# Kernel tuning notes

Hardware: AMD Instinct MI355X
Metric: run time of the kernel (lower is better)

## Reference

```python
import jax, jax.numpy as jnp
import numpy as np
from jax import lax

B, G, D, S = 1, 2048, 64, 2
H_FULL = 200
H0 = H_FULL // 2 ** (S - 1)
PC_RANGE = (-50.0, -50.0, -4.0, 50.0, 50.0, 4.0)
THRESH = 0.05
CHUNK = 128


def conv3x3(x, w):
    # x: [b,c,h,w], w: [o,i,3,3]
    return lax.conv_general_dilated(x, w, (1, 1), 'SAME',
                                    dimension_numbers=('NCHW', 'OIHW', 'NCHW'))


def instance_norm(x, eps=1e-5):
    mu = x.mean(axis=(2, 3), keepdims=True)
    var = x.var(axis=(2, 3), keepdims=True)
    return (x - mu) / jnp.sqrt(var + eps)


def basic_block(x, w1, w2):
    # conv-(BN@init=identity)-relu-conv-(BN)-add-relu
    h = jax.nn.relu(conv3x3(x, w1))
    h = conv3x3(h, w2)
    return jax.nn.relu(x + h)


def upsampling_add(x, skip, w):
    b, c, h, wd = x.shape
    xu = jax.image.resize(x, (b, c, 2 * h, 2 * wd), method='bilinear')
    xu = instance_norm(conv3x3(xu, w))
    return xu + skip


def render_stage(means, cov6, feats, opac, mask, H, W):
    # Orthographic BEV splatting (3DGS-style EWA + front-to-back compositing).
    g, d = feats.shape
    sh = H / 100.0
    sw = W / 100.0
    # full_proj_transform: px = -sh*y + H/2 ; py = -sw*x + W/2
    u = -sh * means[:, 1] + 0.5 * H
    v = -sw * means[:, 0] + 0.5 * W
    # cov2d = J Sigma J^T + 0.3*I, J = [[0,-sh,0],[-sw,0,0]]
    a = sh * sh * cov6[:, 3] + 0.3
    c = sw * sw * cov6[:, 0] + 0.3
    bb = sh * sw * cov6[:, 1]
    det = jnp.maximum(a * c - bb * bb, 1e-8)
    A = c / det
    Bc = -bb / det
    C = a / det
    xs = jnp.arange(W, dtype=jnp.float32)
    ys = jnp.arange(H, dtype=jnp.float32)
    nc = g // CHUNK

    def step(carry, inp):
        T, out = carry
        u_, v_, A_, B_, C_, op_, mk_, ft_ = inp
        dx = u_[:, None, None] - xs[None, None, :]
        dy = v_[:, None, None] - ys[None, :, None]
        power = (-0.5 * (A_[:, None, None] * dx * dx + C_[:, None, None] * dy * dy)
                 - B_[:, None, None] * dx * dy)
        alpha = jnp.minimum(op_[:, None, None] * jnp.exp(power), 0.99)
        alpha = jnp.where((alpha >= 1.0 / 255.0) & mk_[:, None, None] & (power <= 0.0),
                          alpha, 0.0)
        cp = jnp.cumprod(1.0 - alpha, axis=0)
        t_exc = jnp.concatenate([jnp.ones_like(cp[:1]), cp[:-1]], 0) * T
        out = out + jnp.einsum('ghw,gd->dhw', alpha * t_exc, ft_)
        return (T * cp[-1], out), None

    ch = lambda arr: arr.reshape(nc, CHUNK, *arr.shape[1:])
    init = (jnp.ones((H, W), jnp.float32), jnp.zeros((d, H, W), jnp.float32))
    (_, out), _ = lax.scan(step, init,
                           (ch(u), ch(v), ch(A), ch(Bc), ch(C), ch(opac), ch(mask), ch(feats)))
    return out  # bg color = 0


def setup_inputs() -> dict:
    key = jax.random.key(0)
    ks = jax.random.split(key, 10)
    features = jax.random.normal(ks[0], (B, G, D), jnp.float32)
    xy = jax.random.uniform(ks[1], (B, G, 2), jnp.float32, -55.0, 55.0)
    z = jax.random.uniform(ks[2], (B, G, 1), jnp.float32, -5.0, 5.0)
    means3D = jnp.concatenate([xy, z], -1)
    L = jax.random.normal(ks[3], (B, G, 3, 3), jnp.float32) * 0.5
    Sig = jnp.einsum('bgij,bgkj->bgik', L, L) + 0.1 * jnp.eye(3, dtype=jnp.float32)
    cov3D = jnp.stack([Sig[..., 0, 0], Sig[..., 0, 1], Sig[..., 0, 2],
                       Sig[..., 1, 1], Sig[..., 1, 2], Sig[..., 2, 2]], -1)
    opacities = jax.random.uniform(ks[4], (B, G, S), jnp.float32)
    w_scale = 1.0 / np.sqrt(D * 9)
    bev_emb = jax.random.normal(ks[5], (H0 * H0, D), jnp.float32) * 0.02
    conv1_w = jax.random.normal(ks[6], (S, D, D, 3, 3), jnp.float32) * w_scale
    blk_w = jax.random.normal(ks[7], (S, 2, 2, D, D, 3, 3), jnp.float32) * w_scale
    up_w = jax.random.normal(ks[8], (S - 1, D, D, 3, 3), jnp.float32) * w_scale
    return {'features': features, 'means3D': means3D, 'cov3D': cov3D,
            'opacities': opacities, 'bev_emb': bev_emb, 'conv1_w': conv1_w,
            'blk_w': blk_w, 'up_w': up_w}


def reference(features, means3D, cov3D, opacities, bev_emb, conv1_w, blk_w, up_w):
    b = features.shape[0]
    d = features.shape[-1]
    m = means3D
    mask_pos = ((m[..., 0] >= PC_RANGE[0]) & (m[..., 0] <= PC_RANGE[3]) &
                (m[..., 1] >= PC_RANGE[1]) & (m[..., 1] <= PC_RANGE[4]) &
                (m[..., 2] >= PC_RANGE[2]) & (m[..., 2] <= PC_RANGE[5]))
    num_g = jnp.float32(0.0)
    bevs = []
    for s in range(S):
        H = H0 * 2 ** s
        mask = (opacities[..., s] > THRESH) & mask_pos
        rend = jax.vmap(lambda mn, cv, ft, op, mk: render_stage(mn, cv, ft, op, mk, H, H))
        bevs.append(rend(means3D, cov3D, features, opacities[..., s], mask))
        num_g = num_g + jnp.mean(jnp.sum(mask.astype(jnp.float32), 1))
    x = jnp.broadcast_to(jnp.transpose(bev_emb.reshape(H0, H0, d), (2, 0, 1))[None],
                         (b, d, H0, H0))
    for s in range(S):
        bev = conv3x3(bevs[s], conv1_w[s])
        if s == 0:
            x = x + bev
        else:
            x = upsampling_add(x, bev, up_w[s - 1])
        for blk in range(2):
            x = basic_block(x, blk_w[s, blk, 0], blk_w[s, blk, 1])
    return x, num_g
```

## Files before the change

### kernel.cpp

```cpp
#include <hip/hip_runtime.h>
#include <math.h>

#define G_N 2048
#define CCH 256
#define PSTR 12
#define NBLK 1024
#define WC (64 * 64 * 9)

typedef short bhalf8 __attribute__((ext_vector_type(8)));
typedef float f32x4 __attribute__((ext_vector_type(4)));
typedef unsigned short u16;

__device__ __forceinline__ u16 f2bf(float f) {
    unsigned u = __float_as_uint(f);
    unsigned r = (u + 0x7fffu + ((u >> 16) & 1u)) >> 16;
    return (u16)r;
}
__device__ __forceinline__ float b2f(u16 h) {
    return __uint_as_float((unsigned)h << 16);
}

__device__ __forceinline__ ushort4 chload4(const u16* p) {
    unsigned long long u = __hip_atomic_load((const unsigned long long*)p,
        __ATOMIC_RELAXED, __HIP_MEMORY_SCOPE_AGENT);
    union { unsigned long long u; ushort4 s; } x; x.u = u;
    return x.s;
}
__device__ __forceinline__ void chstore4(u16* p, ushort4 v) {
    union { unsigned long long u; ushort4 s; } x; x.s = v;
    __hip_atomic_store((unsigned long long*)p, x.u,
                       __ATOMIC_RELAXED, __HIP_MEMORY_SCOPE_AGENT);
}
__device__ __forceinline__ void cstore8(float* p, float a, float b) {
    union { unsigned long long u; float f[2]; } x;
    x.f[0] = a; x.f[1] = b;
    __hip_atomic_store((unsigned long long*)p, x.u,
                       __ATOMIC_RELAXED, __HIP_MEMORY_SCOPE_AGENT);
}
__device__ __forceinline__ float cload(const float* p) {
    return __hip_atomic_load(p, __ATOMIC_RELAXED, __HIP_MEMORY_SCOPE_AGENT);
}

__device__ __forceinline__ void gbar(int* leaf, int* root, int* flag, int phase) {
    asm volatile("s_waitcnt vmcnt(0) lgkmcnt(0)" ::: "memory");
    __syncthreads();
    if (threadIdx.x == 0) {
        int g = blockIdx.x >> 5;
        int old = atomicAdd(&leaf[g * 16], 1);
        if ((old & 31) == 31) {
            int o2 = atomicAdd(root, 1);
            if ((o2 & 31) == 31)
                __hip_atomic_store(flag, phase, __ATOMIC_RELAXED,
                                   __HIP_MEMORY_SCOPE_AGENT);
        }
        while (__hip_atomic_load(flag, __ATOMIC_RELAXED,
                                 __HIP_MEMORY_SCOPE_AGENT) < phase)
            __builtin_amdgcn_s_sleep(16);
    }
    __syncthreads();
    asm volatile("" ::: "memory");
}

__device__ __forceinline__ void render_tile(
    int unit, const float* __restrict__ params, const int* __restrict__ counts,
    const float* __restrict__ feats, u16* __restrict__ out0,
    u16* __restrict__ out1, char* smem)
{
    int s = (unit < 169) ? 0 : 1;
    int t = (s == 0) ? unit : unit - 169;
    int tw = (s == 0) ? 13 : 25;
    int bxx = t % tw, byy = t / tw;
    int H = 100 << s;
    const float* P = params + s * G_N * PSTR;
    u16* out = s ? out1 : out0;
    int cnt = counts[s];

    float* raw = (float*)smem;
    float* cmp = raw + CCH * PSTR;
    int* s_wsum = (int*)(smem + 24576);

    int tid = threadIdx.x;
    int w = tid >> 6, lane = tid & 63;
    int pxl = lane & 7, pyl = lane >> 3;
    int x0 = bxx * 8, y0 = byy * 8;
    int px = x0 + pxl, py = y0 + pyl;
    bool active = (px < H) && (py < H);
    float fx = (float)px, fy = (float)py;
    float tx0 = (float)x0, tx1 = (float)min(H - 1, x0 + 7);
    float ty0 = (float)y0, ty1 = (float)min(H - 1, y0 + 7);

    f32x4 acc[4];
#pragma unroll
    for (int k = 0; k < 4; ++k) acc[k] = (f32x4){0.f, 0.f, 0.f, 0.f};
    float T = 1.f;

    for (int base = 0; base < cnt; base += CCH) {
        int anyalive = __syncthreads_or((int)(active && T > 1e-6f));
        if (!anyalive) break;
        int n = min(CCH, cnt - base);
        for (int i = tid; i < n * 3; i += 256)
            ((float4*)raw)[i] = ((const float4*)(P + base * PSTR))[i];
        __syncthreads();
        bool pass = false;
        if (tid < n) {
            float u = raw[tid * PSTR + 0], v = raw[tid * PSTR + 1];
            float rx = raw[tid * PSTR + 8], ry = raw[tid * PSTR + 9];
            pass = (u + rx >= tx0) && (u - rx <= tx1) &&
                   (v + ry >= ty0) && (v - ry <= ty1);
        }
        unsigned long long bal = __ballot(pass);
        int prefix = __popcll(bal & ((1ull << lane) - 1ull));
        if (lane == 0) s_wsum[w] = __popcll(bal);
        __syncthreads();
        int woff = 0;
        for (int k = 0; k < 4; ++k) if (k < w) woff += s_wsum[k];
        if (pass) {
            float4* dst = (float4*)(cmp + (woff + prefix) * PSTR);
            const float4* src = (const float4*)(raw + tid * PSTR);
            dst[0] = src[0]; dst[1] = src[1]; dst[2] = src[2];
        }
        __syncthreads();
        int nc = s_wsum[0] + s_wsum[1] + s_wsum[2] + s_wsum[3];
        if (active && T > 1e-6f) {
            for (int j = 0; j < nc; ++j) {
                float4 q0 = *(const float4*)(cmp + j * PSTR);
                float4 q1 = *(const float4*)(cmp + j * PSTR + 4);
                float dx = q0.x - fx, dy = q0.y - fy;
                float power = -0.5f * (q0.z * dx * dx + q1.x * dy * dy) - q0.w * dx * dy;
                if (power <= 0.f && power >= q1.z) {
                    float alpha = fminf(q1.y * __expf(power), 0.99f);
                    float wgt = alpha * T;
                    const f32x4* f4 = (const f32x4*)(feats + __float_as_int(q1.w) * 64) + w * 4;
#pragma unroll
                    for (int k = 0; k < 4; ++k) {
                        f32x4 fv = f4[k];
                        acc[k][0] = fmaf(wgt, fv[0], acc[k][0]);
                        acc[k][1] = fmaf(wgt, fv[1], acc[k][1]);
                        acc[k][2] = fmaf(wgt, fv[2], acc[k][2]);
                        acc[k][3] = fmaf(wgt, fv[3], acc[k][3]);
                    }
                    T *= (1.f - alpha);
                }
            }
        }
    }

    __syncthreads();
    float* shf = (float*)smem;
#pragma unroll
    for (int k = 0; k < 4; ++k)
        *(float4*)&shf[lane * 68 + w * 16 + k * 4] =
            (float4){acc[k][0], acc[k][1], acc[k][2], acc[k][3]};
    __syncthreads();
    for (int j = tid; j < 1024; j += 256) {
        int lp = j >> 4, c4 = (j & 15) * 4;
        int gy = y0 + (lp >> 3), gx = x0 + (lp & 7);
        if (gy < H && gx < H) {
            float4 v = *(float4*)&shf[lp * 68 + c4];
            ushort4 o = { f2bf(v.x), f2bf(v.y), f2bf(v.z), f2bf(v.w) };
            chstore4(&out[((gy * H + gx) << 6) + c4], o);
        }
    }
}

__device__ __forceinline__ void conv_tile(
    int bx, int H, const u16* __restrict__ in, const u16* __restrict__ wp,
    const float* __restrict__ bev, u16* __restrict__ outb,
    int ups, int dostats, float* __restrict__ sacc, char* smem)
{
    u16* xlds = (u16*)smem;
    u16* fin  = (u16*)(smem + 14400);
    float* red = (float*)(smem + 16384 + 8704);

    int tid = threadIdx.x;
    int gw = (H + 7) >> 3;
    int by = bx / gw, bxx = bx - by * gw;
    int y0 = by * 8, x0 = bxx * 8;
    int w = tid >> 6, lane = tid & 63;
    int n = lane & 15, q = lane >> 4;
    int Hh = H >> 1;
    int oy = (y0 >> 1) - 2, ox = (x0 >> 1) - 2;

    if (ups) {
        for (int i = tid; i < 1024; i += 256) {
            int px = i >> 4, c4 = (i & 15) * 4;
            int iy = px >> 3, ix = px & 7;
            int gyi = oy + iy, gxi = ox + ix;
            ushort4 v = {0, 0, 0, 0};
            if (gyi >= 0 && gyi < Hh && gxi >= 0 && gxi < Hh)
                v = chload4(&in[((gyi * Hh + gxi) << 6) + c4]);
            *(ushort4*)&fin[px * 68 + c4] = v;
        }
        __syncthreads();
    }

    for (int i = tid; i < 1600; i += 256) {
        int px = i >> 4, c4 = (i & 15) * 4;
        int yy = px / 10, xx = px - yy * 10;
        int gy = y0 - 1 + yy, gx = x0 - 1 + xx;
        ushort4 v = {0, 0, 0, 0};
        if (gy >= 0 && gy < H && gx >= 0 && gx < H) {
            if (ups) {
                int yi = gy >> 1, xi = gx >> 1;
                int yb = (gy & 1) ? min(yi + 1, Hh - 1) : max(yi - 1, 0);
                int xb = (gx & 1) ? min(xi + 1, Hh - 1) : max(xi - 1, 0);
                int t0 = yi - oy, t1 = xi - ox, t2 = yb - oy, t3 = xb - ox;
                ushort4 f00 = *(const ushort4*)&fin[(t0 * 8 + t1) * 68 + c4];
                ushort4 f01 = *(const ushort4*)&fin[(t0 * 8 + t3) * 68 + c4];
                ushort4 f10 = *(const ushort4*)&fin[(t2 * 8 + t1) * 68 + c4];
                ushort4 f11 = *(const ushort4*)&fin[(t2 * 8 + t3) * 68 + c4];
                v.x = f2bf(0.5625f * b2f(f00.x) + 0.1875f * (b2f(f01.x) + b2f(f10.x)) + 0.0625f * b2f(f11.x));
                v.y = f2bf(0.5625f * b2f(f00.y) + 0.1875f * (b2f(f01.y) + b2f(f10.y)) + 0.0625f * b2f(f11.y));
                v.z = f2bf(0.5625f * b2f(f00.z) + 0.1875f * (b2f(f01.z) + b2f(f10.z)) + 0.0625f * b2f(f11.z));
                v.w = f2bf(0.5625f * b2f(f00.w) + 0.1875f * (b2f(f01.w) + b2f(f10.w)) + 0.0625f * b2f(f11.w));
            } else {
                v = chload4(&in[((gy * H + gx) << 6) + c4]);
            }
        }
        *(ushort4*)&xlds[px * 72 + c4] = v;
    }
    __syncthreads();

    f32x4 acc[4];
#pragma unroll
    for (int m = 0; m < 4; ++m) acc[m] = (f32x4){0.f, 0.f, 0.f, 0.f};
    const bhalf8* wp8 = (const bhalf8*)wp;
    int sy = 2 * w + (n >> 3), sx = n & 7;

    bhalf8 a0 = wp8[0 * 64 + lane];
    bhalf8 a1 = wp8[1 * 64 + lane];
    bhalf8 a2 = wp8[2 * 64 + lane];
    bhalf8 a3 = wp8[3 * 64 + lane];
    bhalf8 bb = *(const bhalf8*)&xlds[(sy * 10 + sx) * 72 + q * 8];

#pragma unroll 1
    for (int p = 0; p < 18; ++p) {
        bhalf8 na0, na1, na2, na3, nbb;
        if (p < 17) {
            int pn = p + 1;
            na0 = wp8[(pn * 4 + 0) * 64 + lane];
            na1 = wp8[(pn * 4 + 1) * 64 + lane];
            na2 = wp8[(pn * 4 + 2) * 64 + lane];
            na3 = wp8[(pn * 4 + 3) * 64 + lane];
            int tap = pn >> 1, ch = pn & 1;
            int dy = tap / 3, dx = tap - dy * 3;
            nbb = *(const bhalf8*)&xlds[((sy + dy) * 10 + sx + dx) * 72 + ch * 32 + q * 8];
        }
        acc[0] = __builtin_amdgcn_mfma_f32_16x16x32_bf16(a0, bb, acc[0], 0, 0, 0);
        acc[1] = __builtin_amdgcn_mfma_f32_16x16x32_bf16(a1, bb, acc[1], 0, 0, 0);
        acc[2] = __builtin_amdgcn_mfma_f32_16x16x32_bf16(a2, bb, acc[2], 0, 0, 0);
        acc[3] = __builtin_amdgcn_mfma_f32_16x16x32_bf16(a3, bb, acc[3], 0, 0, 0);
        a0 = na0; a1 = na1; a2 = na2; a3 = na3; bb = nbb;
    }

    int gy = y0 + sy, gx = x0 + sx;
    if (gy < H && gx < H) {
        int base = (gy * H + gx) << 6;
#pragma unroll
        for (int m = 0; m < 4; ++m) {
            int oc0 = m * 16 + q * 4;
            float v0 = acc[m][0], v1 = acc[m][1], v2 = acc[m][2], v3 = acc[m][3];
            if (bev) {
                float4 av = *(const float4*)&bev[base + oc0];
                v0 += av.x; v1 += av.y; v2 += av.z; v3 += av.w;
            }
            ushort4 o = { f2bf(v0), f2bf(v1), f2bf(v2), f2bf(v3) };
            chstore4(&outb[base + oc0], o);
        }
    }

    if (dostats) {
#pragma unroll
        for (int m = 0; m < 4; ++m)
#pragma unroll
            for (int r = 0; r < 4; ++r) {
                float v = acc[m][r];
                float s = v, s2 = v * v;
#pragma unroll
                for (int d = 1; d < 16; d <<= 1) {
                    s += __shfl_xor(s, d, 64);
                    s2 += __shfl_xor(s2, d, 64);
                }
                if (n == 0) {
                    int oc = m * 16 + q * 4 + r;
                    red[w * 128 + oc] = s;
                    red[w * 128 + 64 + oc] = s2;
                }
            }
        __syncthreads();
        if (tid < 128) {
            float t = red[tid] + red[128 + tid] + red[256 + tid] + red[384 + tid];
            atomicAdd(&sacc[tid], t);
        }
    }
}

__device__ __forceinline__ void bb_tile(
    int bx, int H, const u16* __restrict__ in,
    const u16* __restrict__ wp1, const u16* __restrict__ wp2,
    u16* __restrict__ outb, float* __restrict__ outf, int final_,
    int nrm, const u16* __restrict__ nskip, const float* __restrict__ sraw,
    char* smem)
{
    u16* xin  = (u16*)smem;
    u16* ilds = (u16*)(smem + 20736);
    float* nm = (float*)(smem + 35136);
    float* nr = nm + 64;

    int tid = threadIdx.x;
    int gw = (H + 7) >> 3;
    int by = bx / gw, bxx = bx - by * gw;
    int y0 = by * 8, x0 = bxx * 8;
    int w = tid >> 6, lane = tid & 63;
    int n = lane & 15, q = lane >> 4;

    if (nrm) {
        if (tid < 64) {
            float s = cload(&sraw[tid]), s2 = cload(&sraw[64 + tid]);
            float mean = s * (1.f / 40000.f);
            float var = s2 * (1.f / 40000.f) - mean * mean;
            nm[tid] = mean;
            nr[tid] = rsqrtf(var + 1e-5f);
        }
        __syncthreads();
    }

    for (int i = tid; i < 2304; i += 256) {
        int px = i >> 4, c4 = (i & 15) * 4;
        int yy = px / 12, xx = px - yy * 12;
        int gy = y0 - 2 + yy, gx = x0 - 2 + xx;
        ushort4 v = {0, 0, 0, 0};
        if (gy >= 0 && gy < H && gx >= 0 && gx < H) {
            int off = ((gy * H + gx) << 6) + c4;
            if (nrm) {
                ushort4 a = chload4(&in[off]);
                ushort4 b = chload4(&nskip[off]);
                v.x = f2bf((b2f(a.x) - nm[c4 + 0]) * nr[c4 + 0] + b2f(b.x));
                v.y = f2bf((b2f(a.y) - nm[c4 + 1]) * nr[c4 + 1] + b2f(b.y));
                v.z = f2bf((b2f(a.z) - nm[c4 + 2]) * nr[c4 + 2] + b2f(b.z));
                v.w = f2bf((b2f(a.w) - nm[c4 + 3]) * nr[c4 + 3] + b2f(b.w));
            } else {
                v = chload4(&in[off]);
            }
        }
        *(ushort4*)&xin[px * 72 + c4] = v;
    }
    __syncthreads();

    const bhalf8* w1 = (const bhalf8*)wp1;
#pragma unroll 1
    for (int r = 0; r < 2; ++r) {
        int t = w + 4 * r;
        int px = t * 16 + n;
        bool val = px < 100;
        int pc = val ? px : 0;
        int yy = pc / 10, xx = pc - yy * 10;

        f32x4 acc[4];
#pragma unroll
        for (int m = 0; m < 4; ++m) acc[m] = (f32x4){0.f, 0.f, 0.f, 0.f};

        bhalf8 a0 = w1[0 * 64 + lane];
        bhalf8 a1 = w1[1 * 64 + lane];
        bhalf8 a2 = w1[2 * 64 + lane];
        bhalf8 a3 = w1[3 * 64 + lane];
        bhalf8 bb = *(const bhalf8*)&xin[(yy * 12 + xx) * 72 + q * 8];

#pragma unroll 1
        for (int p = 0; p < 18; ++p) {
            bhalf8 na0, na1, na2, na3, nbb;
            if (p < 17) {
                int pn = p + 1;
                na0 = w1[(pn * 4 + 0) * 64 + lane];
                na1 = w1[(pn * 4 + 1) * 64 + lane];
                na2 = w1[(pn * 4 + 2) * 64 + lane];
                na3 = w1[(pn * 4 + 3) * 64 + lane];
                int tap = pn >> 1, ch = pn & 1;
                int dy = tap / 3, dx = tap - dy * 3;
                nbb = *(const bhalf8*)&xin[((yy + dy) * 12 + xx + dx) * 72 + ch * 32 + q * 8];
            }
            acc[0] = __builtin_amdgcn_mfma_f32_16x16x32_bf16(a0, bb, acc[0], 0, 0, 0);
            acc[1] = __builtin_amdgcn_mfma_f32_16x16x32_bf16(a1, bb, acc[1], 0, 0, 0);
            acc[2] = __builtin_amdgcn_mfma_f32_16x16x32_bf16(a2, bb, acc[2], 0, 0, 0);
            acc[3] = __builtin_amdgcn_mfma_f32_16x16x32_bf16(a3, bb, acc[3], 0, 0, 0);
            a0 = na0; a1 = na1; a2 = na2; a3 = na3; bb = nbb;
        }

        int iy = y0 - 1 + yy, ix = x0 - 1 + xx;
        bool ok = val && iy >= 0 && iy < H && ix >= 0 && ix < H;
        if (val) {
#pragma unroll
            for (int m = 0; m < 4; ++m) {
                ushort4 o = {0, 0, 0, 0};
                if (ok) {
                    o.x = f2bf(fmaxf(acc[m][0], 0.f));
                    o.y = f2bf(fmaxf(acc[m][1], 0.f));
                    o.z = f2bf(fmaxf(acc[m][2], 0.f));
                    o.w = f2bf(fmaxf(acc[m][3], 0.f));
                }
                *(ushort4*)&ilds[px * 72 + m * 16 + q * 4] = o;
            }
        }
    }
    __syncthreads();

    f32x4 acc[4];
#pragma unroll
    for (int m = 0; m < 4; ++m) acc[m] = (f32x4){0.f, 0.f, 0.f, 0.f};
    const bhalf8* w2 = (const bhalf8*)wp2;
    int sy = 2 * w + (n >> 3), sx = n & 7;

    bhalf8 a0 = w2[0 * 64 + lane];
    bhalf8 a1 = w2[1 * 64 + lane];
    bhalf8 a2 = w2[2 * 64 + lane];
    bhalf8 a3 = w2[3 * 64 + lane];
    bhalf8 bb = *(const bhalf8*)&ilds[(sy * 10 + sx) * 72 + q * 8];

#pragma unroll 1
    for (int p = 0; p < 18; ++p) {
        bhalf8 na0, na1, na2, na3, nbb;
        if (p < 17) {
            int pn = p + 1;
            na0 = w2[(pn * 4 + 0) * 64 + lane];
            na1 = w2[(pn * 4 + 1) * 64 + lane];
            na2 = w2[(pn * 4 + 2) * 64 + lane];
            na3 = w2[(pn * 4 + 3) * 64 + lane];
            int tap = pn >> 1, ch = pn & 1;
            int dy = tap / 3, dx = tap - dy * 3;
            nbb = *(const bhalf8*)&ilds[((sy + dy) * 10 + sx + dx) * 72 + ch * 32 + q * 8];
        }
        acc[0] = __builtin_amdgcn_mfma_f32_16x16x32_bf16(a0, bb, acc[0], 0, 0, 0);
        acc[1] = __builtin_amdgcn_mfma_f32_16x16x32_bf16(a1, bb, acc[1], 0, 0, 0);
        acc[2] = __builtin_amdgcn_mfma_f32_16x16x32_bf16(a2, bb, acc[2], 0, 0, 0);
        acc[3] = __builtin_amdgcn_mfma_f32_16x16x32_bf16(a3, bb, acc[3], 0, 0, 0);
        a0 = na0; a1 = na1; a2 = na2; a3 = na3; bb = nbb;
    }

    int gy = y0 + sy, gx = x0 + sx;
    if (gy < H && gx < H) {
        int base = (gy * H + gx) << 6;
#pragma unroll
        for (int m = 0; m < 4; ++m) {
            int oc0 = m * 16 + q * 4;
            ushort4 xr = *(const ushort4*)&xin[((sy + 2) * 12 + sx + 2) * 72 + oc0];
            float v0 = fmaxf(acc[m][0] + b2f(xr.x), 0.f);
            float v1 = fmaxf(acc[m][1] + b2f(xr.y), 0.f);
            float v2 = fmaxf(acc[m][2] + b2f(xr.z), 0.f);
            float v3 = fmaxf(acc[m][3] + b2f(xr.w), 0.f);
            if (final_) {
                int pix = gy * H + gx;
                outf[(oc0 + 0) * H * H + pix] = v0;
                outf[(oc0 + 1) * H * H + pix] = v1;
                outf[(oc0 + 2) * H * H + pix] = v2;
                outf[(oc0 + 3) * H * H + pix] = v3;
            } else {
                ushort4 o = { f2bf(v0), f2bf(v1), f2bf(v2), f2bf(v3) };
                chstore4(&outb[base + oc0], o);
            }
        }
    }
}

__global__ __launch_bounds__(256, 4) void gls_mega(
    const float* __restrict__ feats, const float* __restrict__ bev_emb,
    const float* __restrict__ conv1_w, const float* __restrict__ blk_w,
    const float* __restrict__ up_w, const float* __restrict__ means,
    const float* __restrict__ cov6, const float* __restrict__ opac,
    u16* __restrict__ wprep, float* __restrict__ params, int* __restrict__ cnts,
    u16* __restrict__ R0h, u16* __restrict__ X0h,
    u16* __restrict__ X1h, u16* __restrict__ X2h,
    u16* __restrict__ Qr0h, u16* __restrict__ Sh,
    u16* __restrict__ Uh, u16* __restrict__ Y1h,
    float* __restrict__ out, int* __restrict__ barmem, float* __restrict__ sacc)
{
    __shared__ __align__(16) char smem[36352];
    int bid = blockIdx.x;
    int tid = threadIdx.x;
    int* leaf = barmem;
    int* root = barmem + 512;
    int* flag = barmem + 513;
    int ph = 0;

    if (bid < 2) {
        int s = bid;
        int* s_base = (int*)smem;
        int* s_wsum = s_base + 16;
        if (tid == 0) *s_base = 0;
        __syncthreads();
        float* P = params + s * G_N * PSTR;
        float H = (float)(100 << s);
        float sh = (float)(1 << s);
        for (int it = 0; it < G_N / 256; ++it) {
            int g = it * 256 + tid;
            float mx = means[g * 3 + 0], my = means[g * 3 + 1], mz = means[g * 3 + 2];
            float op = opac[g * 2 + s];
            bool mask = (mx >= -50.f && mx <= 50.f && my >= -50.f && my <= 50.f &&
                         mz >= -4.f && mz <= 4.f && op > 0.05f);
            unsigned long long bal = __ballot(mask);
            int lane = tid & 63, wid = tid >> 6;
            int prefix = __popcll(bal & ((1ull << lane) - 1ull));
            if (lane == 0) s_wsum[wid] = __popcll(bal);
            __syncthreads();
            int woff = 0;
            for (int w = 0; w < 4; ++w) if (w < wid) woff += s_wsum[w];
            int pos = *s_base + woff + prefix;
            if (mask) {
                float u = -sh * my + 0.5f * H;
                float v = -sh * mx + 0.5f * H;
                float a = sh * sh * cov6[g * 6 + 3] + 0.3f;
                float c = sh * sh * cov6[g * 6 + 0] + 0.3f;
                float bb = sh * sh * cov6[g * 6 + 1];
                float det = fmaxf(a * c - bb * bb, 1e-8f);
                float t = logf(255.f * op);
                float* Q = P + pos * PSTR;
                cstore8(&Q[0], u, v);
                cstore8(&Q[2], c / det, -bb / det);
                cstore8(&Q[4], a / det, op);
                cstore8(&Q[6], -t, __int_as_float(g));
                cstore8(&Q[8], sqrtf(2.f * t * a), sqrtf(2.f * t * c));
            }
            __syncthreads();
            if (tid == 0) *s_base += s_wsum[0] + s_wsum[1] + s_wsum[2] + s_wsum[3];
            __syncthreads();
        }
        if (tid == 0)
            __hip_atomic_store(&cnts[s], *s_base, __ATOMIC_RELAXED,
                               __HIP_MEMORY_SCOPE_AGENT);
    }
    gbar(leaf, root, flag, ++ph);

    if (bid < 794) {
        render_tile(bid, params, cnts, feats, R0h, Qr0h, smem);
    } else if (bid < 992) {
        int rb = bid - 794;
        int p = rb % 18, c = rb / 18;
        const float* src;
        if (c == 0) src = conv1_w;
        else if (c <= 4) src = blk_w + (c - 1) * WC;
        else if (c == 5) src = conv1_w + WC;
        else if (c == 6) src = up_w;
        else src = blk_w + (c - 3) * WC;
        int tap = p >> 1;
        int m = tid >> 6, lane = tid & 63;
        int oc = m * 16 + (lane & 15);
        int ci0 = (p & 1) * 32 + (lane >> 4) * 8;
        u16 v[8];
#pragma unroll
        for (int j = 0; j < 8; ++j)
            v[j] = f2bf(src[(oc * 64 + ci0 + j) * 9 + tap]);
        u16* dst = wprep + ((c * 18 + p) * 4 + m) * 64 * 8 + lane * 8;
        chstore4(dst, (ushort4){v[0], v[1], v[2], v[3]});
        chstore4(dst + 4, (ushort4){v[4], v[5], v[6], v[7]});
    }
    gbar(leaf, root, flag, ++ph);

    if (bid < 169)
        conv_tile(bid, 100, R0h, wprep + 0 * WC, bev_emb, X0h, 0, 0, nullptr, smem);
    else if (bid < 794)
        conv_tile(bid - 169, 200, Qr0h, wprep + 5 * WC, nullptr, Sh, 0, 0, nullptr, smem);
    gbar(leaf, root, flag, ++ph);

    if (bid < 169)
        bb_tile(bid, 100, X0h, wprep + 1 * WC, wprep + 2 * WC, X1h,
                nullptr, 0, 0, nullptr, nullptr, smem);
    gbar(leaf, root, flag, ++ph);
    if (bid < 169)
        bb_tile(bid, 100, X1h, wprep + 3 * WC, wprep + 4 * WC, X2h,
                nullptr, 0, 0, nullptr, nullptr, smem);
    gbar(leaf, root, flag, ++ph);

    if (bid < 625)
        conv_tile(bid, 200, X2h, wprep + 6 * WC, nullptr, Uh, 1, 1, sacc, smem);
    gbar(leaf, root, flag, ++ph);

    if (bid < 625)
        bb_tile(bid, 200, Uh, wprep + 7 * WC, wprep + 8 * WC, Y1h,
                nullptr, 0, 1, Sh, sacc, smem);
    gbar(leaf, root, flag, ++ph);

    if (bid == 0 && threadIdx.x == 0)
        out[2560000] = (float)(cnts[0] + cnts[1]);
    if (bid < 625)
        bb_tile(bid, 200, Y1h, wprep + 9 * WC, wprep + 10 * WC, nullptr,
                out, 1, 0, nullptr, nullptr, smem);
}

extern "C" void kernel_launch(void* const* d_in, const int* in_sizes, int n_in,
                              void* d_out, int out_size, void* d_ws, size_t ws_size,
                              hipStream_t stream)
{
    const float* feats   = (const float*)d_in[0];
    const float* means   = (const float*)d_in[1];
    const float* cov6    = (const float*)d_in[2];
    const float* opac    = (const float*)d_in[3];
    const float* bev_emb = (const float*)d_in[4];
    const float* conv1_w = (const float*)d_in[5];
    const float* blk_w   = (const float*)d_in[6];
    const float* up_w    = (const float*)d_in[7];
    float* out = (float*)d_out;
    float* ws = (float*)d_ws;

    float* P      = ws;
    int*   cnts   = (int*)(ws + 49152);
    int*   barmem = (int*)(ws + 49280);
    float* sacc   = ws + 49856;
    u16*   wprep  = (u16*)(ws + 50176);

    u16* R0h  = (u16*)(ws + 262144);
    u16* X0h  = (u16*)(ws + 589824);
    u16* X1h  = (u16*)(ws + 917504);
    u16* X2h  = (u16*)(ws + 1245184);
    u16* Qr0h = (u16*)(ws + 1572864);
    u16* Sh   = (u16*)(ws + 2883584);
    u16* Uh   = (u16*)(ws + 4194304);
    u16* Y1h  = (u16*)(ws + 5505024);

    hipMemsetAsync(barmem, 0, (520 + 64 + 128) * 4, stream);
    gls_mega<<<NBLK, 256, 0, stream>>>(feats, bev_emb, conv1_w, blk_w, up_w,
                                       means, cov6, opac, wprep, P, cnts,
                                       R0h, X0h, X1h, X2h, Qr0h, Sh, Uh, Y1h,
                                       out, barmem, sacc);
    (void)in_sizes; (void)n_in; (void)out_size; (void)ws_size;
}
```

Baseline: 269.2 us.

## Parallelize gaussian preprocessing, drop compaction, rebalance stage-1 conv across phases

Gaussian preprocessing moves from two serial blocks with prefix-sum compaction to 16 blocks that each write one parameter slot per gaussian, with masked ones given a negative radius so the tile culling rejects them. The counts come from atomics. The stage-1 conv1 tiles move out of the stage-0 conv phase and are split across the two stage-0 residual-block phases to balance the work between barriers. Halo loads switch from 8-byte atomic loads to plain 16-byte vector loads, and the memset now also clears the counts. The renderer now scans all 2048 slots instead of only the compacted ones, so it does more culling work per tile.

```diff
diff --git a/kernel.cpp b/kernel.cpp
--- a/kernel.cpp
+++ b/kernel.cpp
@@ -20,12 +20,6 @@
     return __uint_as_float((unsigned)h << 16);
 }
 
-__device__ __forceinline__ ushort4 chload4(const u16* p) {
-    unsigned long long u = __hip_atomic_load((const unsigned long long*)p,
-        __ATOMIC_RELAXED, __HIP_MEMORY_SCOPE_AGENT);
-    union { unsigned long long u; ushort4 s; } x; x.u = u;
-    return x.s;
-}
 __device__ __forceinline__ void chstore4(u16* p, ushort4 v) {
     union { unsigned long long u; ushort4 s; } x; x.s = v;
     __hip_atomic_store((unsigned long long*)p, x.u,
@@ -38,6 +32,9 @@
                        __ATOMIC_RELAXED, __HIP_MEMORY_SCOPE_AGENT);
 }
 __device__ __forceinline__ float cload(const float* p) {
+    return __hip_atomic_load(p, __ATOMIC_RELAXED, __HIP_MEMORY_SCOPE_AGENT);
+}
+__device__ __forceinline__ int iload(const int* p) {
     return __hip_atomic_load(p, __ATOMIC_RELAXED, __HIP_MEMORY_SCOPE_AGENT);
 }
 
@@ -62,7 +59,7 @@
 }
 
 __device__ __forceinline__ void render_tile(
-    int unit, const float* __restrict__ params, const int* __restrict__ counts,
+    int unit, const float* __restrict__ params,
     const float* __restrict__ feats, u16* __restrict__ out0,
     u16* __restrict__ out1, char* smem)
 {
@@ -73,7 +70,6 @@
     int H = 100 << s;
     const float* P = params + s * G_N * PSTR;
     u16* out = s ? out1 : out0;
-    int cnt = counts[s];
 
     float* raw = (float*)smem;
     float* cmp = raw + CCH * PSTR;
@@ -81,9 +77,8 @@
 
     int tid = threadIdx.x;
     int w = tid >> 6, lane = tid & 63;
-    int pxl = lane & 7, pyl = lane >> 3;
     int x0 = bxx * 8, y0 = byy * 8;
-    int px = x0 + pxl, py = y0 + pyl;
+    int px = x0 + (lane & 7), py = y0 + (lane >> 3);
     bool active = (px < H) && (py < H);
     float fx = (float)px, fy = (float)py;
     float tx0 = (float)x0, tx1 = (float)min(H - 1, x0 + 7);
@@ -94,20 +89,16 @@
     for (int k = 0; k < 4; ++k) acc[k] = (f32x4){0.f, 0.f, 0.f, 0.f};
     float T = 1.f;
 
-    for (int base = 0; base < cnt; base += CCH) {
+    for (int base = 0; base < G_N; base += CCH) {
         int anyalive = __syncthreads_or((int)(active && T > 1e-6f));
         if (!anyalive) break;
-        int n = min(CCH, cnt - base);
-        for (int i = tid; i < n * 3; i += 256)
+        for (int i = tid; i < CCH * 3; i += 256)
             ((float4*)raw)[i] = ((const float4*)(P + base * PSTR))[i];
         __syncthreads();
-        bool pass = false;
-        if (tid < n) {
-            float u = raw[tid * PSTR + 0], v = raw[tid * PSTR + 1];
-            float rx = raw[tid * PSTR + 8], ry = raw[tid * PSTR + 9];
-            pass = (u + rx >= tx0) && (u - rx <= tx1) &&
-                   (v + ry >= ty0) && (v - ry <= ty1);
-        }
+        float u = raw[tid * PSTR + 0], v = raw[tid * PSTR + 1];
+        float rx = raw[tid * PSTR + 8], ry = raw[tid * PSTR + 9];
+        bool pass = (u + rx >= tx0) && (u - rx <= tx1) &&
+                    (v + ry >= ty0) && (v - ry <= ty1);
         unsigned long long bal = __ballot(pass);
         int prefix = __popcll(bal & ((1ull << lane) - 1ull));
         if (lane == 0) s_wsum[w] = __popcll(bal);
@@ -170,7 +161,7 @@
 {
     u16* xlds = (u16*)smem;
     u16* fin  = (u16*)(smem + 14400);
-    float* red = (float*)(smem + 16384 + 8704);
+    float* red = (float*)(smem + 25600);
 
     int tid = threadIdx.x;
     int gw = (H + 7) >> 3;
@@ -182,42 +173,47 @@
     int oy = (y0 >> 1) - 2, ox = (x0 >> 1) - 2;
 
     if (ups) {
-        for (int i = tid; i < 1024; i += 256) {
-            int px = i >> 4, c4 = (i & 15) * 4;
+        for (int i = tid; i < 512; i += 256) {
+            int px = i >> 3, c8 = (i & 7) * 8;
             int iy = px >> 3, ix = px & 7;
             int gyi = oy + iy, gxi = ox + ix;
+            uint4 v = {0, 0, 0, 0};
+            if (gyi >= 0 && gyi < Hh && gxi >= 0 && gxi < Hh)
+                v = *(const uint4*)&in[((gyi * Hh + gxi) << 6) + c8];
+            *(uint4*)&fin[px * 72 + c8] = v;
+        }
+        __syncthreads();
+        for (int i = tid; i < 1600; i += 256) {
+            int px = i >> 4, c4 = (i & 15) * 4;
+            int yy = px / 10, xx = px - yy * 10;
+            int gy = y0 - 1 + yy, gx = x0 - 1 + xx;
             ushort4 v = {0, 0, 0, 0};
-            if (gyi >= 0 && gyi < Hh && gxi >= 0 && gxi < Hh)
-                v = chload4(&in[((gyi * Hh + gxi) << 6) + c4]);
-            *(ushort4*)&fin[px * 68 + c4] = v;
-        }
-        __syncthreads();
-    }
-
-    for (int i = tid; i < 1600; i += 256) {
-        int px = i >> 4, c4 = (i & 15) * 4;
-        int yy = px / 10, xx = px - yy * 10;
-        int gy = y0 - 1 + yy, gx = x0 - 1 + xx;
-        ushort4 v = {0, 0, 0, 0};
-        if (gy >= 0 && gy < H && gx >= 0 && gx < H) {
-            if (ups) {
+            if (gy >= 0 && gy < H && gx >= 0 && gx < H) {
                 int yi = gy >> 1, xi = gx >> 1;
                 int yb = (gy & 1) ? min(yi + 1, Hh - 1) : max(yi - 1, 0);
                 int xb = (gx & 1) ? min(xi + 1, Hh - 1) : max(xi - 1, 0);
                 int t0 = yi - oy, t1 = xi - ox, t2 = yb - oy, t3 = xb - ox;
-                ushort4 f00 = *(const ushort4*)&fin[(t0 * 8 + t1) * 68 + c4];
-                ushort4 f01 = *(const ushort4*)&fin[(t0 * 8 + t3) * 68 + c4];
-                ushort4 f10 = *(const ushort4*)&fin[(t2 * 8 + t1) * 68 + c4];
-                ushort4 f11 = *(const ushort4*)&fin[(t2 * 8 + t3) * 68 + c4];
+                ushort4 f00 = *(const ushort4*)&fin[(t0 * 8 + t1) * 72 + c4];
+                ushort4 f01 = *(const ushort4*)&fin[(t0 * 8 + t3) * 72 + c4];
+                ushort4 f10 = *(const ushort4*)&fin[(t2 * 8 + t1) * 72 + c4];
+                ushort4 f11 = *(const ushort4*)&fin[(t2 * 8 + t3) * 72 + c4];
                 v.x = f2bf(0.5625f * b2f(f00.x) + 0.1875f * (b2f(f01.x) + b2f(f10.x)) + 0.0625f * b2f(f11.x));
                 v.y = f2bf(0.5625f * b2f(f00.y) + 0.1875f * (b2f(f01.y) + b2f(f10.y)) + 0.0625f * b2f(f11.y));
                 v.z = f2bf(0.5625f * b2f(f00.z) + 0.1875f * (b2f(f01.z) + b2f(f10.z)) + 0.0625f * b2f(f11.z));
                 v.w = f2bf(0.5625f * b2f(f00.w) + 0.1875f * (b2f(f01.w) + b2f(f10.w)) + 0.0625f * b2f(f11.w));
-            } else {
-                v = chload4(&in[((gy * H + gx) << 6) + c4]);
-            }
-        }
-        *(ushort4*)&xlds[px * 72 + c4] = v;
+            }
+            *(ushort4*)&xlds[px * 72 + c4] = v;
+        }
+    } else {
+        for (int i = tid; i < 800; i += 256) {
+            int px = i >> 3, c8 = (i & 7) * 8;
+            int yy = px / 10, xx = px - yy * 10;
+            int gy = y0 - 1 + yy, gx = x0 - 1 + xx;
+            uint4 v = {0, 0, 0, 0};
+            if (gy >= 0 && gy < H && gx >= 0 && gx < H)
+                v = *(const uint4*)&in[((gy * H + gx) << 6) + c8];
+            *(uint4*)&xlds[px * 72 + c8] = v;
+        }
     }
     __syncthreads();
 
@@ -323,27 +319,32 @@
             nr[tid] = rsqrtf(var + 1e-5f);
         }
         __syncthreads();
-    }
-
-    for (int i = tid; i < 2304; i += 256) {
-        int px = i >> 4, c4 = (i & 15) * 4;
-        int yy = px / 12, xx = px - yy * 12;
-        int gy = y0 - 2 + yy, gx = x0 - 2 + xx;
-        ushort4 v = {0, 0, 0, 0};
-        if (gy >= 0 && gy < H && gx >= 0 && gx < H) {
-            int off = ((gy * H + gx) << 6) + c4;
-            if (nrm) {
-                ushort4 a = chload4(&in[off]);
-                ushort4 b = chload4(&nskip[off]);
+        for (int i = tid; i < 2304; i += 256) {
+            int px = i >> 4, c4 = (i & 15) * 4;
+            int yy = px / 12, xx = px - yy * 12;
+            int gy = y0 - 2 + yy, gx = x0 - 2 + xx;
+            ushort4 v = {0, 0, 0, 0};
+            if (gy >= 0 && gy < H && gx >= 0 && gx < H) {
+                int off = ((gy * H + gx) << 6) + c4;
+                ushort4 a = *(const ushort4*)&in[off];
+                ushort4 b = *(const ushort4*)&nskip[off];
                 v.x = f2bf((b2f(a.x) - nm[c4 + 0]) * nr[c4 + 0] + b2f(b.x));
                 v.y = f2bf((b2f(a.y) - nm[c4 + 1]) * nr[c4 + 1] + b2f(b.y));
                 v.z = f2bf((b2f(a.z) - nm[c4 + 2]) * nr[c4 + 2] + b2f(b.z));
                 v.w = f2bf((b2f(a.w) - nm[c4 + 3]) * nr[c4 + 3] + b2f(b.w));
-            } else {
-                v = chload4(&in[off]);
-            }
-        }
-        *(ushort4*)&xin[px * 72 + c4] = v;
+            }
+            *(ushort4*)&xin[px * 72 + c4] = v;
+        }
+    } else {
+        for (int i = tid; i < 1152; i += 256) {
+            int px = i >> 3, c8 = (i & 7) * 8;
+            int yy = px / 12, xx = px - yy * 12;
+            int gy = y0 - 2 + yy, gx = x0 - 2 + xx;
+            uint4 v = {0, 0, 0, 0};
+            if (gy >= 0 && gy < H && gx >= 0 && gx < H)
+                v = *(const uint4*)&in[((gy * H + gx) << 6) + c8];
+            *(uint4*)&xin[px * 72 + c8] = v;
+        }
     }
     __syncthreads();
 
@@ -481,56 +482,41 @@
     int* flag = barmem + 513;
     int ph = 0;
 
-    if (bid < 2) {
-        int s = bid;
-        int* s_base = (int*)smem;
-        int* s_wsum = s_base + 16;
-        if (tid == 0) *s_base = 0;
-        __syncthreads();
-        float* P = params + s * G_N * PSTR;
-        float H = (float)(100 << s);
-        float sh = (float)(1 << s);
-        for (int it = 0; it < G_N / 256; ++it) {
-            int g = it * 256 + tid;
-            float mx = means[g * 3 + 0], my = means[g * 3 + 1], mz = means[g * 3 + 2];
-            float op = opac[g * 2 + s];
-            bool mask = (mx >= -50.f && mx <= 50.f && my >= -50.f && my <= 50.f &&
-                         mz >= -4.f && mz <= 4.f && op > 0.05f);
-            unsigned long long bal = __ballot(mask);
-            int lane = tid & 63, wid = tid >> 6;
-            int prefix = __popcll(bal & ((1ull << lane) - 1ull));
-            if (lane == 0) s_wsum[wid] = __popcll(bal);
-            __syncthreads();
-            int woff = 0;
-            for (int w = 0; w < 4; ++w) if (w < wid) woff += s_wsum[w];
-            int pos = *s_base + woff + prefix;
-            if (mask) {
-                float u = -sh * my + 0.5f * H;
-                float v = -sh * mx + 0.5f * H;
-                float a = sh * sh * cov6[g * 6 + 3] + 0.3f;
-                float c = sh * sh * cov6[g * 6 + 0] + 0.3f;
-                float bb = sh * sh * cov6[g * 6 + 1];
-                float det = fmaxf(a * c - bb * bb, 1e-8f);
-                float t = logf(255.f * op);
-                float* Q = P + pos * PSTR;
-                cstore8(&Q[0], u, v);
-                cstore8(&Q[2], c / det, -bb / det);
-                cstore8(&Q[4], a / det, op);
-                cstore8(&Q[6], -t, __int_as_float(g));
-                cstore8(&Q[8], sqrtf(2.f * t * a), sqrtf(2.f * t * c));
-            }
-            __syncthreads();
-            if (tid == 0) *s_base += s_wsum[0] + s_wsum[1] + s_wsum[2] + s_wsum[3];
-            __syncthreads();
-        }
-        if (tid == 0)
-            __hip_atomic_store(&cnts[s], *s_base, __ATOMIC_RELAXED,
-                               __HIP_MEMORY_SCOPE_AGENT);
+    if (bid < 16) {
+        int item = bid * 256 + tid;
+        int s = item >> 11, g = item & 2047;
+        float mx = means[g * 3 + 0], my = means[g * 3 + 1], mz = means[g * 3 + 2];
+        float op = opac[g * 2 + s];
+        bool mask = (mx >= -50.f && mx <= 50.f && my >= -50.f && my <= 50.f &&
+                     mz >= -4.f && mz <= 4.f && op > 0.05f);
+        float Hs = (float)(100 << s), sh = (float)(1 << s);
+        float u = 0.f, v = 0.f, A = 0.f, B = 0.f, C = 0.f, pthr = 0.f;
+        float rx = -1.f, ry = -1.f;
+        if (mask) {
+            u = -sh * my + 0.5f * Hs;
+            v = -sh * mx + 0.5f * Hs;
+            float a = sh * sh * cov6[g * 6 + 3] + 0.3f;
+            float c = sh * sh * cov6[g * 6 + 0] + 0.3f;
+            float bb = sh * sh * cov6[g * 6 + 1];
+            float det = fmaxf(a * c - bb * bb, 1e-8f);
+            float t = logf(255.f * op);
+            A = c / det; B = -bb / det; C = a / det;
+            pthr = -t;
+            rx = sqrtf(2.f * t * a); ry = sqrtf(2.f * t * c);
+        }
+        float* Q = params + (s * G_N + g) * PSTR;
+        cstore8(&Q[0], u, v);
+        cstore8(&Q[2], A, B);
+        cstore8(&Q[4], C, op);
+        cstore8(&Q[6], pthr, __int_as_float(g));
+        cstore8(&Q[8], rx, ry);
+        unsigned long long bal = __ballot(mask);
+        if ((tid & 63) == 0) atomicAdd(&cnts[s], __popcll(bal));
     }
     gbar(leaf, root, flag, ++ph);
 
     if (bid < 794) {
-        render_tile(bid, params, cnts, feats, R0h, Qr0h, smem);
+        render_tile(bid, params, feats, R0h, Qr0h, smem);
     } else if (bid < 992) {
         int rb = bid - 794;
         int p = rb % 18, c = rb / 18;
@@ -556,17 +542,20 @@
 
     if (bid < 169)
         conv_tile(bid, 100, R0h, wprep + 0 * WC, bev_emb, X0h, 0, 0, nullptr, smem);
-    else if (bid < 794)
-        conv_tile(bid - 169, 200, Qr0h, wprep + 5 * WC, nullptr, Sh, 0, 0, nullptr, smem);
     gbar(leaf, root, flag, ++ph);
 
     if (bid < 169)
         bb_tile(bid, 100, X0h, wprep + 1 * WC, wprep + 2 * WC, X1h,
                 nullptr, 0, 0, nullptr, nullptr, smem);
+    else if (bid < 481)
+        conv_tile(bid - 169, 200, Qr0h, wprep + 5 * WC, nullptr, Sh, 0, 0, nullptr, smem);
     gbar(leaf, root, flag, ++ph);
+
     if (bid < 169)
         bb_tile(bid, 100, X1h, wprep + 3 * WC, wprep + 4 * WC, X2h,
                 nullptr, 0, 0, nullptr, nullptr, smem);
+    else if (bid < 482)
+        conv_tile(312 + bid - 169, 200, Qr0h, wprep + 5 * WC, nullptr, Sh, 0, 0, nullptr, smem);
     gbar(leaf, root, flag, ++ph);
 
     if (bid < 625)
@@ -579,7 +568,7 @@
     gbar(leaf, root, flag, ++ph);
 
     if (bid == 0 && threadIdx.x == 0)
-        out[2560000] = (float)(cnts[0] + cnts[1]);
+        out[2560000] = (float)(iload(&cnts[0]) + iload(&cnts[1]));
     if (bid < 625)
         bb_tile(bid, 200, Y1h, wprep + 9 * WC, wprep + 10 * WC, nullptr,
                 out, 1, 0, nullptr, nullptr, smem);
@@ -615,7 +604,7 @@
     u16* Uh   = (u16*)(ws + 4194304);
     u16* Y1h  = (u16*)(ws + 5505024);
 
-    hipMemsetAsync(barmem, 0, (520 + 64 + 128) * 4, stream);
+    hipMemsetAsync(cnts, 0, (49984 - 49152) * 4, stream);
     gls_mega<<<NBLK, 256, 0, stream>>>(feats, bev_emb, conv1_w, blk_w, up_w,
                                        means, cov6, opac, wprep, P, cnts,
                                        R0h, X0h, X1h, X2h, Qr0h, Sh, Uh, Y1h,
```

Measured after the change: 260.0 us. 1.04x faster.
